# Kernel tuning notes

Measured on AMD Instinct MI355X. Metric: run time of the kernel, lower is better.

Reference implementation:

```python
import jax, jax.numpy as jnp
import numpy as np

N = 100000      # num vertices
NE = 20000      # num hyperedges
NNZ = 1600000   # incidence pairs
NFEAT = 128
NHID = 64       # nhid * nhead = 8 * 8
NCLASS = 40
NLAYER = 4
ALPHA = 0.1
LAMDA = 0.5


def setup_inputs() -> dict:
    key = jax.random.key(0)
    ks = jax.random.split(key, 9)
    x = jax.random.normal(ks[0], (N, NFEAT), dtype=jnp.float32)
    vertex = jax.random.randint(ks[1], (NNZ,), 0, N, dtype=jnp.int32)
    edges = jax.random.randint(ks[2], (NNZ,), 0, NE, dtype=jnp.int32)
    degE = jax.random.uniform(ks[3], (NE, 1), dtype=jnp.float32)
    degV = jax.random.uniform(ks[4], (N, 1), dtype=jnp.float32)
    W0 = jax.random.normal(ks[5], (NFEAT, NHID), dtype=jnp.float32) * 0.05
    b0 = jnp.zeros((NHID,), jnp.float32)
    Ws = jax.random.normal(ks[6], (NLAYER, NHID, NHID), dtype=jnp.float32) * 0.05
    Wout = jax.random.normal(ks[7], (NHID, NCLASS), dtype=jnp.float32) * 0.05
    bout = jnp.zeros((NCLASS,), jnp.float32)
    return dict(x=x, degE=degE, degV=degV, W0=W0, b0=b0, Ws=Ws,
                Wout=Wout, bout=bout, vertex=vertex, edges=edges)


def _normalize_l2(X):
    # torch: norm computed on detached X, inf scales zeroed
    norm = jnp.linalg.norm(jax.lax.stop_gradient(X), axis=1, keepdims=True)
    scale = jnp.where(norm > 0, 1.0 / norm, 0.0)
    return X * scale


def reference(x, degE, degV, W0, b0, Ws, Wout, bout, vertex, edges):
    # per-hyperedge member counts for the 'mean' first_aggregate
    counts = jax.ops.segment_sum(jnp.ones((NNZ,), x.dtype), edges, num_segments=NE)
    counts = jnp.maximum(counts, 1.0)[:, None]  # [NE,1]

    X = jax.nn.relu(x @ W0 + b0)   # [N, NHID]
    X0 = X
    for i in range(NLAYER):
        beta = float(np.log(LAMDA / (i + 1) + 1.0))
        Xve = X[vertex]                                                   # [NNZ, NHID]
        Xe = jax.ops.segment_sum(Xve, edges, num_segments=NE) / counts   # vertex->edge mean
        Xe = Xe * degE                                                    # [NE, NHID]
        Xev = Xe[edges]                                                   # [NNZ, NHID]
        Xv = jax.ops.segment_sum(Xev, vertex, num_segments=N) * degV     # edge->vertex sum
        Xn = _normalize_l2(Xv)                                            # use_norm=True
        Xi = (1.0 - ALPHA) * Xn + ALPHA * X0
        X = jax.nn.relu((1.0 - beta) * Xi + beta * (Xi @ Ws[i]))
    logits = X @ Wout + bout
    return jax.nn.log_softmax(logits, axis=1)
```

## Files before the change

### kernel.cpp

```cpp
#include <hip/hip_runtime.h>
#include <math.h>

constexpr int NV   = 100000;
constexpr int NEg  = 20000;
constexpr int NNZp = 1600000;
constexpr int NF   = 128;
constexpr int NH   = 64;
constexpr int NC   = 40;

constexpr int WE  = 64;
constexpr int NBE = (NEg + WE - 1) / WE;
constexpr int WV  = 256;
constexpr int NBV = (NV + WV - 1) / WV;
constexpr int CAPS = 6400;
constexpr int CH   = 2048;
constexpr int PBLK = (NNZp + CH - 1) / CH;

typedef __bf16 bf16x8 __attribute__((ext_vector_type(8)));
typedef float  f32x4  __attribute__((ext_vector_type(4)));

__device__ __forceinline__ float bf2f(unsigned short u) {
    unsigned int x = ((unsigned int)u) << 16;
    return __builtin_bit_cast(float, x);
}
__device__ __forceinline__ unsigned short f2bf(float f) {
    unsigned int x = __builtin_bit_cast(unsigned int, f);
    x += 0x7fffu + ((x >> 16) & 1u);
    return (unsigned short)(x >> 16);
}
__device__ __forceinline__ ushort4 pack4(float a, float b, float c, float d) {
    ushort4 u; u.x = f2bf(a); u.y = f2bf(b); u.z = f2bf(c); u.w = f2bf(d);
    return u;
}

__global__ __launch_bounds__(256) void coarse_hist(const int* __restrict__ vertex,
                                                   const int* __restrict__ edges,
                                                   int* __restrict__ cnt_be,
                                                   int* __restrict__ cnt_bv) {
    __shared__ int he[NBE], hv[NBV];
    for (int i = threadIdx.x; i < NBE; i += 256) he[i] = 0;
    for (int i = threadIdx.x; i < NBV; i += 256) hv[i] = 0;
    __syncthreads();
    const int base = blockIdx.x * CH;
    const int end  = min(base + CH, NNZp);
    for (int i = base + threadIdx.x; i < end; i += 256) {
        atomicAdd(&he[edges[i]  >> 6], 1);
        atomicAdd(&hv[vertex[i] >> 8], 1);
    }
    __syncthreads();
    for (int i = threadIdx.x; i < NBE; i += 256) if (he[i]) atomicAdd(&cnt_be[i], he[i]);
    for (int i = threadIdx.x; i < NBV; i += 256) if (hv[i]) atomicAdd(&cnt_bv[i], hv[i]);
}

__global__ __launch_bounds__(512) void scan_buckets(const int* __restrict__ cnt_be,
                                                    const int* __restrict__ cnt_bv,
                                                    int* __restrict__ rsb_e,
                                                    int* __restrict__ rsb_v,
                                                    int* __restrict__ rs_e,
                                                    int* __restrict__ rs_v) {
    __shared__ int s[512];
    const int n      = (blockIdx.x == 0) ? NBE : NBV;
    const int* c     = (blockIdx.x == 0) ? cnt_be : cnt_bv;
    int* r           = (blockIdx.x == 0) ? rsb_e : rsb_v;
    const int t = threadIdx.x;
    int v = (t < n) ? c[t] : 0;
    s[t] = v;
    __syncthreads();
    for (int o = 1; o < 512; o <<= 1) {
        int u = (t >= o) ? s[t - o] : 0;
        __syncthreads();
        s[t] += u;
        __syncthreads();
    }
    if (t < n) r[t] = s[t] - v;
    if (t == 0) {
        r[n] = NNZp;
        if (blockIdx.x == 0) rs_e[NEg] = NNZp;
        else                 rs_v[NV]  = NNZp;
    }
}

__global__ __launch_bounds__(256) void partition_both(const int* __restrict__ vertex,
                                                      const int* __restrict__ edges,
                                                      const int* __restrict__ rsb_e,
                                                      const int* __restrict__ rsb_v,
                                                      int* __restrict__ gcur_e,
                                                      int* __restrict__ gcur_v,
                                                      int* __restrict__ vid_out,
                                                      int* __restrict__ eid_out) {
    __shared__ int se[CH], sv[CH];
    __shared__ int cur_e[NBE], cur_v[NBV];
    const int tid = threadIdx.x;
    for (int i = tid; i < NBE; i += 256) cur_e[i] = 0;
    for (int i = tid; i < NBV; i += 256) cur_v[i] = 0;
    __syncthreads();
    const int base = blockIdx.x * CH;
    const int n    = min(base + CH, NNZp) - base;
    for (int i = tid; i < n; i += 256) {
        int e = edges[base + i];
        int v = vertex[base + i];
        se[i] = e; sv[i] = v;
        atomicAdd(&cur_e[e >> 6], 1);
        atomicAdd(&cur_v[v >> 8], 1);
    }
    __syncthreads();
    for (int i = tid; i < NBE; i += 256) {
        int h = cur_e[i];
        cur_e[i] = rsb_e[i] + (h ? atomicAdd(&gcur_e[i], h) : 0);
    }
    for (int i = tid; i < NBV; i += 256) {
        int h = cur_v[i];
        cur_v[i] = rsb_v[i] + (h ? atomicAdd(&gcur_v[i], h) : 0);
    }
    __syncthreads();
    for (int i = tid; i < n; i += 256) {
        int e = se[i], v = sv[i];
        int pe = atomicAdd(&cur_e[e >> 6], 1);
        vid_out[pe] = (v << 6) | (e & 63);
        int pv = atomicAdd(&cur_v[v >> 8], 1);
        eid_out[pv] = (e << 8) | (v & 255);
    }
}

__global__ __launch_bounds__(512) void local_sort_both(const int* __restrict__ rsb_e,
                                                       const int* __restrict__ rsb_v,
                                                       int* __restrict__ vid_buf,
                                                       int* __restrict__ eid_buf,
                                                       int* __restrict__ rs_e,
                                                       int* __restrict__ rs_v,
                                                       const float* __restrict__ degE,
                                                       float* __restrict__ scaleE) {
    __shared__ int stage[CAPS];
    __shared__ int hist[256], off[256], cnt2[256];
    const bool eside = blockIdx.x < NBE;
    const int b   = eside ? blockIdx.x : blockIdx.x - NBE;
    const int W   = eside ? 64 : 256;
    const int FB  = eside ? 6 : 8;
    const int NID = eside ? NEg : NV;
    const int* rsb = eside ? rsb_e : rsb_v;
    int* buf       = eside ? vid_buf : eid_buf;
    int* rs        = eside ? rs_e : rs_v;
    const int base = rsb[b];
    const int sz   = rsb[b + 1] - base;
    const int tid = threadIdx.x;
    if (tid < 256) { hist[tid] = 0; cnt2[tid] = 0; }
    __syncthreads();
    for (int t = tid; t < sz; t += 512) atomicAdd(&hist[buf[base + t] & (W - 1)], 1);
    __syncthreads();
    {
        int v = (tid < W) ? hist[tid] : 0;
        if (tid < W) off[tid] = v;
        __syncthreads();
        for (int o = 1; o < W; o <<= 1) {
            int u = (tid < W && tid >= o) ? off[tid - o] : 0;
            __syncthreads();
            if (tid < W) off[tid] += u;
            __syncthreads();
        }
        if (tid < W) off[tid] -= v;
    }
    if (tid < W) {
        int gid = b * W + tid;
        if (gid < NID) {
            rs[gid] = base + off[tid];
            if (eside) {
                int c = hist[tid];
                scaleE[gid] = degE[gid] / (float)(c < 1 ? 1 : c);
            }
        }
    }
    __syncthreads();
    for (int t = tid; t < sz; t += 512) {
        int w = buf[base + t];
        int f = w & (W - 1);
        int rk = off[f] + atomicAdd(&cnt2[f], 1);
        stage[rk] = w >> FB;
    }
    __syncthreads();
    for (int t = tid; t < sz; t += 512) buf[base + t] = stage[t];
}

__global__ __launch_bounds__(256) void make_wfrag(const float* __restrict__ Ws,
                                                  const float* __restrict__ Wout,
                                                  const float* __restrict__ W0,
                                                  unsigned short* __restrict__ frag) {
    int t = blockIdx.x * 256 + threadIdx.x;
    int lane = t & 63;
    int g = t >> 6;
    int quad = lane >> 4, cl = lane & 15;
    unsigned short o[8];
    if (g < 32) {
        int li = g >> 3, w = (g >> 1) & 3, kh = g & 1;
        int n = w * 16 + cl;
#pragma unroll
        for (int j = 0; j < 8; ++j) {
            int k = kh * 32 + quad * 8 + j;
            o[j] = f2bf(Ws[(size_t)li * NH * NH + k * NH + n]);
        }
    } else if (g < 40) {
        int w = (g - 32) >> 1, kh = g & 1;
        int n = w * 16 + cl;
#pragma unroll
        for (int j = 0; j < 8; ++j) {
            int k = kh * 32 + quad * 8 + j;
            o[j] = (n < NC) ? f2bf(Wout[k * NC + n]) : (unsigned short)0;
        }
    } else {
        int w = (g - 40) >> 2, kb = (g - 40) & 3;
        int n = w * 16 + cl;
#pragma unroll
        for (int j = 0; j < 8; ++j) {
            int k = kb * 32 + quad * 8 + j;
            o[j] = f2bf(W0[k * NH + n]);
        }
    }
    unsigned short* dst = frag + (size_t)g * 512 + lane * 8;
    *((ushort4*)dst)       = *(ushort4*)&o[0];
    *((ushort4*)(dst + 4)) = *(ushort4*)&o[4];
}

__global__ __launch_bounds__(256) void gemm0_kernel(const float* __restrict__ x,
                                                    const unsigned short* __restrict__ W0frag,
                                                    const float* __restrict__ b0,
                                                    unsigned short* __restrict__ Xbf,
                                                    unsigned short* __restrict__ X0bf) {
    __shared__ unsigned short xs[16][136];
    const int tid = threadIdx.x;
    const int r  = tid >> 4;
    const int c8 = (tid & 15) * 8;
    const int rowbase = blockIdx.x * 16;
    float4 p0 = *((const float4*)(x + (size_t)(rowbase + r) * NF + c8));
    float4 p1 = *((const float4*)(x + (size_t)(rowbase + r) * NF + c8 + 4));
    *((ushort4*)&xs[r][c8])     = pack4(p0.x, p0.y, p0.z, p0.w);
    *((ushort4*)&xs[r][c8 + 4]) = pack4(p1.x, p1.y, p1.z, p1.w);
    __syncthreads();
    const int lane = tid & 63;
    const int wv   = tid >> 6;
    const int quad = lane >> 4;
    const int cl   = lane & 15;
    f32x4 acc = {0.f, 0.f, 0.f, 0.f};
#pragma unroll
    for (int kb = 0; kb < 4; ++kb) {
        bf16x8 a = *((const bf16x8*)&xs[cl][kb * 32 + quad * 8]);
        bf16x8 b = *((const bf16x8*)(W0frag + ((size_t)(wv * 4 + kb) * 64 + lane) * 8));
        acc = __builtin_amdgcn_mfma_f32_16x16x32_bf16(a, b, acc, 0, 0, 0);
    }
    const int col = wv * 16 + cl;
    const float bo = b0[col];
#pragma unroll
    for (int p = 0; p < 4; ++p) {
        const int orow = quad * 4 + p;
        float o = acc[p] + bo;
        o = o > 0.f ? o : 0.f;
        unsigned short ob = f2bf(o);
        const size_t idx = (size_t)(rowbase + orow) * NH + col;
        Xbf[idx]  = ob;
        X0bf[idx] = ob;
    }
}

__global__ __launch_bounds__(256) void gather_ve(const int* __restrict__ rs_e,
                                                 const int* __restrict__ vid_sorted,
                                                 const unsigned short* __restrict__ Xbf,
                                                 const float* __restrict__ scaleE,
                                                 unsigned short* __restrict__ Xebf) {
    const int tid = threadIdx.x;
    const int l16 = tid & 15;
    const int e = blockIdx.x * 16 + (tid >> 4);
    const int b  = rs_e[e];
    const int en = rs_e[e + 1];
    const float s = scaleE[e];
    float ax = 0.f, ay = 0.f, az = 0.f, aw = 0.f;
    int m = b;
    if (m + 4 <= en) {
        int i0 = vid_sorted[m], i1 = vid_sorted[m + 1];
        int i2 = vid_sorted[m + 2], i3 = vid_sorted[m + 3];
        m += 4;
        while (m + 4 <= en) {
            int j0 = vid_sorted[m], j1 = vid_sorted[m + 1];
            int j2 = vid_sorted[m + 2], j3 = vid_sorted[m + 3];
            m += 4;
            ushort4 p = *((const ushort4*)(Xbf + (size_t)i0 * NH) + l16);
            ushort4 q = *((const ushort4*)(Xbf + (size_t)i1 * NH) + l16);
            ushort4 u = *((const ushort4*)(Xbf + (size_t)i2 * NH) + l16);
            ushort4 t = *((const ushort4*)(Xbf + (size_t)i3 * NH) + l16);
            ax += bf2f(p.x) + bf2f(q.x) + bf2f(u.x) + bf2f(t.x);
            ay += bf2f(p.y) + bf2f(q.y) + bf2f(u.y) + bf2f(t.y);
            az += bf2f(p.z) + bf2f(q.z) + bf2f(u.z) + bf2f(t.z);
            aw += bf2f(p.w) + bf2f(q.w) + bf2f(u.w) + bf2f(t.w);
            i0 = j0; i1 = j1; i2 = j2; i3 = j3;
        }
        ushort4 p = *((const ushort4*)(Xbf + (size_t)i0 * NH) + l16);
        ushort4 q = *((const ushort4*)(Xbf + (size_t)i1 * NH) + l16);
        ushort4 u = *((const ushort4*)(Xbf + (size_t)i2 * NH) + l16);
        ushort4 t = *((const ushort4*)(Xbf + (size_t)i3 * NH) + l16);
        ax += bf2f(p.x) + bf2f(q.x) + bf2f(u.x) + bf2f(t.x);
        ay += bf2f(p.y) + bf2f(q.y) + bf2f(u.y) + bf2f(t.y);
        az += bf2f(p.z) + bf2f(q.z) + bf2f(u.z) + bf2f(t.z);
        aw += bf2f(p.w) + bf2f(q.w) + bf2f(u.w) + bf2f(t.w);
    }
    for (; m < en; ++m) {
        ushort4 p = *((const ushort4*)(Xbf + (size_t)vid_sorted[m] * NH) + l16);
        ax += bf2f(p.x); ay += bf2f(p.y); az += bf2f(p.z); aw += bf2f(p.w);
    }
    *((ushort4*)(Xebf + (size_t)e * NH) + l16) = pack4(ax * s, ay * s, az * s, aw * s);
}

template <bool LAST>
__global__ __launch_bounds__(256) void gather_ev_update(const int* __restrict__ rs_v,
                                                        const int* __restrict__ eid_sorted,
                                                        const unsigned short* __restrict__ Xebf,
                                                        const float* __restrict__ degV,
                                                        const unsigned short* __restrict__ X0bf,
                                                        const unsigned short* __restrict__ WfragL,
                                                        unsigned short* __restrict__ Xbf,
                                                        float beta,
                                                        const unsigned short* __restrict__ WfragH,
                                                        const float* __restrict__ bout,
                                                        float* __restrict__ outp) {
    __shared__ unsigned short xis_bf[16][72];
    __shared__ unsigned short xo_bf[LAST ? 16 * 72 : 1];
    __shared__ float lg[LAST ? 16 * 48 : 1];
    const int tid = threadIdx.x;
    const int l16 = tid & 15;
    const int r   = tid >> 4;
    const int v = blockIdx.x * 16 + r;
    const int b  = rs_v[v];
    const int en = rs_v[v + 1];
    const float dv = degV[v];
    float ax = 0.f, ay = 0.f, az = 0.f, aw = 0.f;
    int m = b;
    if (m + 4 <= en) {
        int i0 = eid_sorted[m], i1 = eid_sorted[m + 1];
        int i2 = eid_sorted[m + 2], i3 = eid_sorted[m + 3];
        m += 4;
        while (m + 4 <= en) {
            int j0 = eid_sorted[m], j1 = eid_sorted[m + 1];
            int j2 = eid_sorted[m + 2], j3 = eid_sorted[m + 3];
            m += 4;
            ushort4 p = *((const ushort4*)(Xebf + (size_t)i0 * NH) + l16);
            ushort4 q = *((const ushort4*)(Xebf + (size_t)i1 * NH) + l16);
            ushort4 u = *((const ushort4*)(Xebf + (size_t)i2 * NH) + l16);
            ushort4 t = *((const ushort4*)(Xebf + (size_t)i3 * NH) + l16);
            ax += bf2f(p.x) + bf2f(q.x) + bf2f(u.x) + bf2f(t.x);
            ay += bf2f(p.y) + bf2f(q.y) + bf2f(u.y) + bf2f(t.y);
            az += bf2f(p.z) + bf2f(q.z) + bf2f(u.z) + bf2f(t.z);
            aw += bf2f(p.w) + bf2f(q.w) + bf2f(u.w) + bf2f(t.w);
            i0 = j0; i1 = j1; i2 = j2; i3 = j3;
        }
        ushort4 p = *((const ushort4*)(Xebf + (size_t)i0 * NH) + l16);
        ushort4 q = *((const ushort4*)(Xebf + (size_t)i1 * NH) + l16);
        ushort4 u = *((const ushort4*)(Xebf + (size_t)i2 * NH) + l16);
        ushort4 t = *((const ushort4*)(Xebf + (size_t)i3 * NH) + l16);
        ax += bf2f(p.x) + bf2f(q.x) + bf2f(u.x) + bf2f(t.x);
        ay += bf2f(p.y) + bf2f(q.y) + bf2f(u.y) + bf2f(t.y);
        az += bf2f(p.z) + bf2f(q.z) + bf2f(u.z) + bf2f(t.z);
        aw += bf2f(p.w) + bf2f(q.w) + bf2f(u.w) + bf2f(t.w);
    }
    for (; m < en; ++m) {
        ushort4 p = *((const ushort4*)(Xebf + (size_t)eid_sorted[m] * NH) + l16);
        ax += bf2f(p.x); ay += bf2f(p.y); az += bf2f(p.z); aw += bf2f(p.w);
    }
    ax *= dv; ay *= dv; az *= dv; aw *= dv;
    float sq = ax * ax + ay * ay + az * az + aw * aw;
#pragma unroll
    for (int o = 1; o < 16; o <<= 1) sq += __shfl_xor(sq, o);
    float norm = sqrtf(sq);
    float inv = norm > 0.f ? 1.f / norm : 0.f;
    ushort4 u0 = *((const ushort4*)(X0bf + (size_t)v * NH) + l16);
    float xi0 = 0.9f * ax * inv + 0.1f * bf2f(u0.x);
    float xi1 = 0.9f * ay * inv + 0.1f * bf2f(u0.y);
    float xi2 = 0.9f * az * inv + 0.1f * bf2f(u0.z);
    float xi3 = 0.9f * aw * inv + 0.1f * bf2f(u0.w);
    *((ushort4*)&xis_bf[r][l16 * 4]) = pack4(xi0, xi1, xi2, xi3);
    __syncthreads();

    const int lane = tid & 63;
    const int wv   = tid >> 6;
    const int quad = lane >> 4;
    const int cl   = lane & 15;
    bf16x8 bw0 = *((const bf16x8*)(WfragL + ((size_t)(wv * 2 + 0) * 64 + lane) * 8));
    bf16x8 bw1 = *((const bf16x8*)(WfragL + ((size_t)(wv * 2 + 1) * 64 + lane) * 8));
    bf16x8 a0 = *((const bf16x8*)&xis_bf[cl][quad * 8]);
    bf16x8 a1 = *((const bf16x8*)&xis_bf[cl][32 + quad * 8]);
    f32x4 acc = {0.f, 0.f, 0.f, 0.f};
    acc = __builtin_amdgcn_mfma_f32_16x16x32_bf16(a0, bw0, acc, 0, 0, 0);
    acc = __builtin_amdgcn_mfma_f32_16x16x32_bf16(a1, bw1, acc, 0, 0, 0);

    const float ob = 1.f - beta;
    const int col = wv * 16 + cl;
#pragma unroll
    for (int p = 0; p < 4; ++p) {
        const int row = quad * 4 + p;
        float xiv = bf2f(xis_bf[row][col]);
        float o = ob * xiv + beta * acc[p];
        o = o > 0.f ? o : 0.f;
        if (!LAST) {
            Xbf[(size_t)(blockIdx.x * 16 + row) * NH + col] = f2bf(o);
        } else {
            xo_bf[row * 72 + col] = f2bf(o);
        }
    }
    if (LAST) {
        __syncthreads();
        bf16x8 bh0 = *((const bf16x8*)(WfragH + ((size_t)(wv * 2 + 0) * 64 + lane) * 8));
        bf16x8 bh1 = *((const bf16x8*)(WfragH + ((size_t)(wv * 2 + 1) * 64 + lane) * 8));
        bf16x8 ah0 = *((const bf16x8*)&xo_bf[cl * 72 + quad * 8]);
        bf16x8 ah1 = *((const bf16x8*)&xo_bf[cl * 72 + 32 + quad * 8]);
        f32x4 acch = {0.f, 0.f, 0.f, 0.f};
        acch = __builtin_amdgcn_mfma_f32_16x16x32_bf16(ah0, bh0, acch, 0, 0, 0);
        acch = __builtin_amdgcn_mfma_f32_16x16x32_bf16(ah1, bh1, acch, 0, 0, 0);
        if (col < NC) {
            float bo = bout[col];
#pragma unroll
            for (int p = 0; p < 4; ++p) lg[(quad * 4 + p) * 48 + col] = acch[p] + bo;
        }
        __syncthreads();
        const int r0 = wv * 4;
        const bool act = lane < NC;
        float a0s = act ? lg[(r0 + 0) * 48 + lane] : -INFINITY;
        float a1s = act ? lg[(r0 + 1) * 48 + lane] : -INFINITY;
        float a2s = act ? lg[(r0 + 2) * 48 + lane] : -INFINITY;
        float a3s = act ? lg[(r0 + 3) * 48 + lane] : -INFINITY;
        float m0 = a0s, m1 = a1s, m2 = a2s, m3 = a3s;
#pragma unroll
        for (int o = 32; o; o >>= 1) {
            m0 = fmaxf(m0, __shfl_xor(m0, o));
            m1 = fmaxf(m1, __shfl_xor(m1, o));
            m2 = fmaxf(m2, __shfl_xor(m2, o));
            m3 = fmaxf(m3, __shfl_xor(m3, o));
        }
        float e0 = act ? expf(a0s - m0) : 0.f;
        float e1 = act ? expf(a1s - m1) : 0.f;
        float e2 = act ? expf(a2s - m2) : 0.f;
        float e3 = act ? expf(a3s - m3) : 0.f;
#pragma unroll
        for (int o = 32; o; o >>= 1) {
            e0 += __shfl_xor(e0, o);
            e1 += __shfl_xor(e1, o);
            e2 += __shfl_xor(e2, o);
            e3 += __shfl_xor(e3, o);
        }
        if (act) {
            const size_t vb = (size_t)(blockIdx.x * 16 + r0) * NC + lane;
            outp[vb + 0 * NC] = a0s - m0 - logf(e0);
            outp[vb + 1 * NC] = a1s - m1 - logf(e1);
            outp[vb + 2 * NC] = a2s - m2 - logf(e2);
            outp[vb + 3 * NC] = a3s - m3 - logf(e3);
        }
    }
}

extern "C" void kernel_launch(void* const* d_in, const int* in_sizes, int n_in,
                              void* d_out, int out_size, void* d_ws, size_t ws_size,
                              hipStream_t stream) {
    const float* x    = (const float*)d_in[0];
    const float* degE = (const float*)d_in[1];
    const float* degV = (const float*)d_in[2];
    const float* W0   = (const float*)d_in[3];
    const float* b0   = (const float*)d_in[4];
    const float* Ws   = (const float*)d_in[5];
    const float* Wout = (const float*)d_in[6];
    const float* bout = (const float*)d_in[7];
    const int* vertex = (const int*)d_in[8];
    const int* edges  = (const int*)d_in[9];
    float* out = (float*)d_out;

    float* scaleE = (float*)d_ws;
    unsigned short* Xbf  = (unsigned short*)(scaleE + NEg);
    unsigned short* X0bf = Xbf + (size_t)NV * NH;
    unsigned short* Xebf = X0bf + (size_t)NV * NH;
    int* cnt_be = (int*)(Xebf + (size_t)NEg * NH);
    int* cnt_bv = cnt_be + NBE;
    int* gcur_e = cnt_bv + NBV;
    int* gcur_v = gcur_e + NBE;
    int* rsb_e  = gcur_v + NBV;
    int* rsb_v  = rsb_e + (NBE + 1);
    int* rs_e   = rsb_v + (NBV + 1);
    int* rs_v   = rs_e + (NEg + 1);
    int* vid_sorted = rs_v + (NV + 1);
    int* eid_sorted = vid_sorted + NNZp;
    unsigned short* Wfrag = (unsigned short*)(eid_sorted + NNZp);

    hipMemsetAsync(cnt_be, 0, (size_t)(NBE + NBV) * 2 * sizeof(int), stream);
    make_wfrag<<<14, 256, 0, stream>>>(Ws, Wout, W0, Wfrag);
    coarse_hist<<<PBLK, 256, 0, stream>>>(vertex, edges, cnt_be, cnt_bv);
    scan_buckets<<<2, 512, 0, stream>>>(cnt_be, cnt_bv, rsb_e, rsb_v, rs_e, rs_v);
    partition_both<<<PBLK, 256, 0, stream>>>(vertex, edges, rsb_e, rsb_v,
                                             gcur_e, gcur_v, vid_sorted, eid_sorted);
    local_sort_both<<<NBE + NBV, 512, 0, stream>>>(rsb_e, rsb_v, vid_sorted, eid_sorted,
                                                   rs_e, rs_v, degE, scaleE);

    gemm0_kernel<<<NV / 16, 256, 0, stream>>>(x, Wfrag + 40 * 512, b0, Xbf, X0bf);

    const float betas[4] = {logf(0.5f / 1.f + 1.f), logf(0.5f / 2.f + 1.f),
                            logf(0.5f / 3.f + 1.f), logf(0.5f / 4.f + 1.f)};

    for (int i = 0; i < 3; ++i) {
        gather_ve<<<NEg / 16, 256, 0, stream>>>(rs_e, vid_sorted, Xbf, scaleE, Xebf);
        gather_ev_update<false><<<NV / 16, 256, 0, stream>>>(rs_v, eid_sorted, Xebf, degV,
                                                             X0bf, Wfrag + (size_t)i * 4096,
                                                             Xbf, betas[i],
                                                             nullptr, nullptr, nullptr);
    }
    gather_ve<<<NEg / 16, 256, 0, stream>>>(rs_e, vid_sorted, Xbf, scaleE, Xebf);
    gather_ev_update<true><<<NV / 16, 256, 0, stream>>>(rs_v, eid_sorted, Xebf, degV,
                                                        X0bf, Wfrag + (size_t)3 * 4096,
                                                        Xbf, betas[3],
                                                        Wfrag + 16384, bout, out);
}
```

Baseline: 451.0 us.

## Fuse histogram, scan and partition into one cooperative kernel with grid sync

Merges the coarse histogram, bucket scan and partition kernels into a single cooperative launch with a grid-wide barrier. Edge and vertex ids stay in registers across the barrier, so the input arrays are read only once. Each block redundantly scans the global bucket counts. Within a block, entries are staged in shared memory by bucket so the global writes become contiguous runs. This saves two launches and one pass over the inputs, but adds grid-sync cost, requires all 391 blocks to be co-resident, and uses more shared memory and registers per block.

```diff
diff --git a/kernel.cpp b/kernel.cpp
--- a/kernel.cpp
+++ b/kernel.cpp
@@ -1,5 +1,8 @@
 #include <hip/hip_runtime.h>
+#include <hip/hip_cooperative_groups.h>
 #include <math.h>
+
+namespace cg = cooperative_groups;
 
 constexpr int NV   = 100000;
 constexpr int NEg  = 20000;
@@ -13,8 +16,8 @@
 constexpr int WV  = 256;
 constexpr int NBV = (NV + WV - 1) / WV;
 constexpr int CAPS = 6400;
-constexpr int CH   = 2048;
-constexpr int PBLK = (NNZp + CH - 1) / CH;
+constexpr int CHB  = 4096;
+constexpr int GB   = (NNZp + CHB - 1) / CHB;
 
 typedef __bf16 bf16x8 __attribute__((ext_vector_type(8)));
 typedef float  f32x4  __attribute__((ext_vector_type(4)));
@@ -33,92 +36,125 @@
     return u;
 }
 
-__global__ __launch_bounds__(256) void coarse_hist(const int* __restrict__ vertex,
-                                                   const int* __restrict__ edges,
-                                                   int* __restrict__ cnt_be,
-                                                   int* __restrict__ cnt_bv) {
-    __shared__ int he[NBE], hv[NBV];
-    for (int i = threadIdx.x; i < NBE; i += 256) he[i] = 0;
-    for (int i = threadIdx.x; i < NBV; i += 256) hv[i] = 0;
-    __syncthreads();
-    const int base = blockIdx.x * CH;
-    const int end  = min(base + CH, NNZp);
-    for (int i = base + threadIdx.x; i < end; i += 256) {
-        atomicAdd(&he[edges[i]  >> 6], 1);
-        atomicAdd(&hv[vertex[i] >> 8], 1);
-    }
-    __syncthreads();
-    for (int i = threadIdx.x; i < NBE; i += 256) if (he[i]) atomicAdd(&cnt_be[i], he[i]);
-    for (int i = threadIdx.x; i < NBV; i += 256) if (hv[i]) atomicAdd(&cnt_bv[i], hv[i]);
-}
-
-__global__ __launch_bounds__(512) void scan_buckets(const int* __restrict__ cnt_be,
-                                                    const int* __restrict__ cnt_bv,
-                                                    int* __restrict__ rsb_e,
-                                                    int* __restrict__ rsb_v,
-                                                    int* __restrict__ rs_e,
-                                                    int* __restrict__ rs_v) {
-    __shared__ int s[512];
-    const int n      = (blockIdx.x == 0) ? NBE : NBV;
-    const int* c     = (blockIdx.x == 0) ? cnt_be : cnt_bv;
-    int* r           = (blockIdx.x == 0) ? rsb_e : rsb_v;
+__device__ __forceinline__ void scan512(const int* src, int m, int* sc) {
     const int t = threadIdx.x;
-    int v = (t < n) ? c[t] : 0;
-    s[t] = v;
+    __syncthreads();
+    sc[t]       = (t < m) ? src[t] : 0;
+    sc[t + 256] = (t + 256 < m) ? src[t + 256] : 0;
     __syncthreads();
     for (int o = 1; o < 512; o <<= 1) {
-        int u = (t >= o) ? s[t - o] : 0;
+        int a = (t >= o) ? sc[t - o] : 0;
+        int b = (t + 256 >= o) ? sc[t + 256 - o] : 0;
         __syncthreads();
-        s[t] += u;
+        sc[t] += a;
+        sc[t + 256] += b;
         __syncthreads();
     }
-    if (t < n) r[t] = s[t] - v;
-    if (t == 0) {
-        r[n] = NNZp;
-        if (blockIdx.x == 0) rs_e[NEg] = NNZp;
-        else                 rs_v[NV]  = NNZp;
-    }
-}
-
-__global__ __launch_bounds__(256) void partition_both(const int* __restrict__ vertex,
-                                                      const int* __restrict__ edges,
-                                                      const int* __restrict__ rsb_e,
-                                                      const int* __restrict__ rsb_v,
-                                                      int* __restrict__ gcur_e,
-                                                      int* __restrict__ gcur_v,
-                                                      int* __restrict__ vid_out,
-                                                      int* __restrict__ eid_out) {
-    __shared__ int se[CH], sv[CH];
-    __shared__ int cur_e[NBE], cur_v[NBV];
+}
+
+__global__ __launch_bounds__(256) void build_coop(const int* __restrict__ vertex,
+                                                  const int* __restrict__ edges,
+                                                  int* __restrict__ cnt_be,
+                                                  int* __restrict__ cnt_bv,
+                                                  int* __restrict__ gcur_e,
+                                                  int* __restrict__ gcur_v,
+                                                  int* __restrict__ rsb_e,
+                                                  int* __restrict__ rsb_v,
+                                                  int* __restrict__ rs_e,
+                                                  int* __restrict__ rs_v,
+                                                  int* __restrict__ vid_out,
+                                                  int* __restrict__ eid_out) {
+    __shared__ int harr_e[NBE], harr_v[NBV];
+    __shared__ int gb[NBV], off[NBV], curr[NBV];
+    __shared__ int sc[512];
+    __shared__ int stage[CHB];
     const int tid = threadIdx.x;
-    for (int i = tid; i < NBE; i += 256) cur_e[i] = 0;
-    for (int i = tid; i < NBV; i += 256) cur_v[i] = 0;
-    __syncthreads();
-    const int base = blockIdx.x * CH;
-    const int n    = min(base + CH, NNZp) - base;
+    const int base = blockIdx.x * CHB;
+    const int n = min(NNZp - base, CHB);
+
+    for (int i = tid; i < NBE; i += 256) harr_e[i] = 0;
+    for (int i = tid; i < NBV; i += 256) harr_v[i] = 0;
+    __syncthreads();
+
+    int re[16], rv[16];
+#pragma unroll
+    for (int j = 0; j < 16; ++j) {
+        int i = j * 256 + tid;
+        bool ok = i < n;
+        re[j] = ok ? edges[base + i] : -1;
+        rv[j] = ok ? vertex[base + i] : -1;
+        if (ok) {
+            atomicAdd(&harr_e[re[j] >> 6], 1);
+            atomicAdd(&harr_v[rv[j] >> 8], 1);
+        }
+    }
+    __syncthreads();
+    for (int i = tid; i < NBE; i += 256) if (harr_e[i]) atomicAdd(&cnt_be[i], harr_e[i]);
+    for (int i = tid; i < NBV; i += 256) if (harr_v[i]) atomicAdd(&cnt_bv[i], harr_v[i]);
+
+    cg::this_grid().sync();
+
+    scan512(cnt_be, NBE, sc);
+    if (blockIdx.x == 0) {
+        for (int k = tid; k < NBE; k += 256) rsb_e[k] = sc[k] - cnt_be[k];
+        if (tid == 0) { rsb_e[NBE] = NNZp; rs_e[NEg] = NNZp; }
+    }
+    for (int k = tid; k < NBE; k += 256) {
+        int h = harr_e[k];
+        gb[k] = (sc[k] - cnt_be[k]) + (h ? atomicAdd(&gcur_e[k], h) : 0);
+    }
+    scan512(harr_e, NBE, sc);
+    for (int k = tid; k < NBE; k += 256) {
+        int o = sc[k] - harr_e[k];
+        off[k] = o; curr[k] = o;
+    }
+    __syncthreads();
+#pragma unroll
+    for (int j = 0; j < 16; ++j) {
+        if (re[j] >= 0) {
+            int k = re[j] >> 6;
+            int p = atomicAdd(&curr[k], 1);
+            stage[p] = (int)(((unsigned)rv[j] << 15) | (unsigned)re[j]);
+        }
+    }
+    __syncthreads();
     for (int i = tid; i < n; i += 256) {
-        int e = edges[base + i];
-        int v = vertex[base + i];
-        se[i] = e; sv[i] = v;
-        atomicAdd(&cur_e[e >> 6], 1);
-        atomicAdd(&cur_v[v >> 8], 1);
-    }
-    __syncthreads();
-    for (int i = tid; i < NBE; i += 256) {
-        int h = cur_e[i];
-        cur_e[i] = rsb_e[i] + (h ? atomicAdd(&gcur_e[i], h) : 0);
-    }
-    for (int i = tid; i < NBV; i += 256) {
-        int h = cur_v[i];
-        cur_v[i] = rsb_v[i] + (h ? atomicAdd(&gcur_v[i], h) : 0);
+        unsigned w = (unsigned)stage[i];
+        int e = (int)(w & 0x7fffu);
+        int k = e >> 6;
+        vid_out[gb[k] + (i - off[k])] = (int)(((w >> 15) << 6) | (unsigned)(e & 63));
+    }
+    __syncthreads();
+
+    scan512(cnt_bv, NBV, sc);
+    if (blockIdx.x == 0) {
+        for (int k = tid; k < NBV; k += 256) rsb_v[k] = sc[k] - cnt_bv[k];
+        if (tid == 0) { rsb_v[NBV] = NNZp; rs_v[NV] = NNZp; }
+    }
+    for (int k = tid; k < NBV; k += 256) {
+        int h = harr_v[k];
+        gb[k] = (sc[k] - cnt_bv[k]) + (h ? atomicAdd(&gcur_v[k], h) : 0);
+    }
+    scan512(harr_v, NBV, sc);
+    for (int k = tid; k < NBV; k += 256) {
+        int o = sc[k] - harr_v[k];
+        off[k] = o; curr[k] = o;
+    }
+    __syncthreads();
+#pragma unroll
+    for (int j = 0; j < 16; ++j) {
+        if (rv[j] >= 0) {
+            int k = rv[j] >> 8;
+            int p = atomicAdd(&curr[k], 1);
+            stage[p] = (int)(((unsigned)re[j] << 17) | (unsigned)rv[j]);
+        }
     }
     __syncthreads();
     for (int i = tid; i < n; i += 256) {
-        int e = se[i], v = sv[i];
-        int pe = atomicAdd(&cur_e[e >> 6], 1);
-        vid_out[pe] = (v << 6) | (e & 63);
-        int pv = atomicAdd(&cur_v[v >> 8], 1);
-        eid_out[pv] = (e << 8) | (v & 255);
+        unsigned w = (unsigned)stage[i];
+        int v = (int)(w & 0x1ffffu);
+        int k = v >> 8;
+        eid_out[gb[k] + (i - off[k])] = (int)(((w >> 17) << 8) | (unsigned)(v & 255));
     }
 }
 
@@ -484,10 +520,12 @@
 
     hipMemsetAsync(cnt_be, 0, (size_t)(NBE + NBV) * 2 * sizeof(int), stream);
     make_wfrag<<<14, 256, 0, stream>>>(Ws, Wout, W0, Wfrag);
-    coarse_hist<<<PBLK, 256, 0, stream>>>(vertex, edges, cnt_be, cnt_bv);
-    scan_buckets<<<2, 512, 0, stream>>>(cnt_be, cnt_bv, rsb_e, rsb_v, rs_e, rs_v);
-    partition_both<<<PBLK, 256, 0, stream>>>(vertex, edges, rsb_e, rsb_v,
-                                             gcur_e, gcur_v, vid_sorted, eid_sorted);
+    {
+        void* args[] = {(void*)&vertex, (void*)&edges, (void*)&cnt_be, (void*)&cnt_bv,
+                        (void*)&gcur_e, (void*)&gcur_v, (void*)&rsb_e, (void*)&rsb_v,
+                        (void*)&rs_e, (void*)&rs_v, (void*)&vid_sorted, (void*)&eid_sorted};
+        hipLaunchCooperativeKernel((void*)build_coop, dim3(GB), dim3(256), args, 0, stream);
+    }
     local_sort_both<<<NBE + NBV, 512, 0, stream>>>(rsb_e, rsb_v, vid_sorted, eid_sorted,
                                                    rs_e, rs_v, degE, scaleE);
 
```

Result: slower. 485.9 us (+7.7%).

## Stage partition scatter through shared memory for coalesced bucket writes

Applied to the files above, without the earlier changes.

The partition kernel now sorts each chunk's entries by coarse bucket in shared memory, using a block-wide scan to find bucket offsets, before writing them to global memory. Entries of the same bucket then go to contiguous global addresses instead of being scattered one at a time. Keys are kept in registers, and the edge and vertex partitions are done one after the other. This adds scan passes and extra barriers per block.

```diff
diff --git a/kernel.cpp b/kernel.cpp
--- a/kernel.cpp
+++ b/kernel.cpp
@@ -31,6 +31,22 @@
 __device__ __forceinline__ ushort4 pack4(float a, float b, float c, float d) {
     ushort4 u; u.x = f2bf(a); u.y = f2bf(b); u.z = f2bf(c); u.w = f2bf(d);
     return u;
+}
+
+__device__ __forceinline__ void scan512(const int* src, int m, int* sc) {
+    const int t = threadIdx.x;
+    __syncthreads();
+    sc[t]       = (t < m) ? src[t] : 0;
+    sc[t + 256] = (t + 256 < m) ? src[t + 256] : 0;
+    __syncthreads();
+    for (int o = 1; o < 512; o <<= 1) {
+        int a = (t >= o) ? sc[t - o] : 0;
+        int b = (t + 256 >= o) ? sc[t + 256 - o] : 0;
+        __syncthreads();
+        sc[t] += a;
+        sc[t + 256] += b;
+        __syncthreads();
+    }
 }
 
 __global__ __launch_bounds__(256) void coarse_hist(const int* __restrict__ vertex,
@@ -88,37 +104,76 @@
                                                       int* __restrict__ gcur_v,
                                                       int* __restrict__ vid_out,
                                                       int* __restrict__ eid_out) {
-    __shared__ int se[CH], sv[CH];
-    __shared__ int cur_e[NBE], cur_v[NBV];
+    __shared__ int h[NBV], gb[NBV], off[NBV], curr[NBV];
+    __shared__ int sc[512];
+    __shared__ int stage[CH];
     const int tid = threadIdx.x;
-    for (int i = tid; i < NBE; i += 256) cur_e[i] = 0;
-    for (int i = tid; i < NBV; i += 256) cur_v[i] = 0;
-    __syncthreads();
     const int base = blockIdx.x * CH;
-    const int n    = min(base + CH, NNZp) - base;
+    const int n = min(NNZp - base, CH);
+    int re[CH / 256], rv[CH / 256];
+#pragma unroll
+    for (int j = 0; j < CH / 256; ++j) {
+        int i = j * 256 + tid;
+        bool ok = i < n;
+        re[j] = ok ? edges[base + i] : -1;
+        rv[j] = ok ? vertex[base + i] : -1;
+    }
+    for (int k = tid; k < NBE; k += 256) h[k] = 0;
+    __syncthreads();
+#pragma unroll
+    for (int j = 0; j < CH / 256; ++j)
+        if (re[j] >= 0) atomicAdd(&h[re[j] >> 6], 1);
+    scan512(h, NBE, sc);
+    for (int k = tid; k < NBE; k += 256) {
+        int hk = h[k];
+        int o = sc[k] - hk;
+        off[k] = o; curr[k] = o;
+        gb[k] = rsb_e[k] + (hk ? atomicAdd(&gcur_e[k], hk) : 0);
+    }
+    __syncthreads();
+#pragma unroll
+    for (int j = 0; j < CH / 256; ++j) {
+        if (re[j] >= 0) {
+            int k = re[j] >> 6;
+            int p = atomicAdd(&curr[k], 1);
+            stage[p] = (int)(((unsigned)rv[j] << 15) | (unsigned)re[j]);
+        }
+    }
+    __syncthreads();
     for (int i = tid; i < n; i += 256) {
-        int e = edges[base + i];
-        int v = vertex[base + i];
-        se[i] = e; sv[i] = v;
-        atomicAdd(&cur_e[e >> 6], 1);
-        atomicAdd(&cur_v[v >> 8], 1);
-    }
-    __syncthreads();
-    for (int i = tid; i < NBE; i += 256) {
-        int h = cur_e[i];
-        cur_e[i] = rsb_e[i] + (h ? atomicAdd(&gcur_e[i], h) : 0);
-    }
-    for (int i = tid; i < NBV; i += 256) {
-        int h = cur_v[i];
-        cur_v[i] = rsb_v[i] + (h ? atomicAdd(&gcur_v[i], h) : 0);
+        unsigned w = (unsigned)stage[i];
+        int e = (int)(w & 0x7fffu);
+        int k = e >> 6;
+        vid_out[gb[k] + (i - off[k])] = (int)(((w >> 15) << 6) | (unsigned)(e & 63));
+    }
+    __syncthreads();
+    for (int k = tid; k < NBV; k += 256) h[k] = 0;
+    __syncthreads();
+#pragma unroll
+    for (int j = 0; j < CH / 256; ++j)
+        if (rv[j] >= 0) atomicAdd(&h[rv[j] >> 8], 1);
+    scan512(h, NBV, sc);
+    for (int k = tid; k < NBV; k += 256) {
+        int hk = h[k];
+        int o = sc[k] - hk;
+        off[k] = o; curr[k] = o;
+        gb[k] = rsb_v[k] + (hk ? atomicAdd(&gcur_v[k], hk) : 0);
+    }
+    __syncthreads();
+#pragma unroll
+    for (int j = 0; j < CH / 256; ++j) {
+        if (rv[j] >= 0) {
+            int k = rv[j] >> 8;
+            int p = atomicAdd(&curr[k], 1);
+            stage[p] = (int)(((unsigned)re[j] << 17) | (unsigned)rv[j]);
+        }
     }
     __syncthreads();
     for (int i = tid; i < n; i += 256) {
-        int e = se[i], v = sv[i];
-        int pe = atomicAdd(&cur_e[e >> 6], 1);
-        vid_out[pe] = (v << 6) | (e & 63);
-        int pv = atomicAdd(&cur_v[v >> 8], 1);
-        eid_out[pv] = (e << 8) | (v & 255);
+        unsigned w = (unsigned)stage[i];
+        int v = (int)(w & 0x1ffffu);
+        int k = v >> 8;
+        eid_out[gb[k] + (i - off[k])] = (int)(((w >> 17) << 8) | (unsigned)(v & 255));
     }
 }
 
```

New measurement: 456.2 us. Within noise of the previous version (+1.2%).
